# Kernel optimization log

Measured on AMD Instinct MI355X. Metric: run time of the kernel, lower is better.

## Reference

```python
import jax, jax.numpy as jnp
import numpy as np

T = 32            # num_tsteps
B = 8192          # batch_size
W_IN0, W_OUT0 = 36, 18
W_IN1, W_OUT1 = 18, 8
TILE0, TILE1 = 2, 1
BETA = (0.95, 0.95)
TH = (0.55, 0.25)
Q = 15000.0       # sephia mrr_Q
ER_DB = 20.0      # sephia extinction ratio
IL_DB = 0.0       # sephia insertion loss
SHIFT_PM = -250.0 # sephia resonance shift per unit spike
P_UNITY = 1e-4    # dbm_to_watt(-10): optical power per WDM channel at unit input


def _lif(inp, mem, beta, th):
    # snntorch Leaky, reset_mechanism='zero', reset_delay=True:
    # reset decided from incoming mem, membrane zeroed before leak+integrate.
    reset = (mem > th).astype(inp.dtype)
    mem_new = (beta * mem + inp) * (1.0 - reset)
    spk = (mem_new > th).astype(inp.dtype)
    return spk, mem_new


def _allpass(spk, wl_nm):
    # All-pass MRR modulator: spike shifts the ring resonance by SHIFT_PM.
    # Normalized detuning delta = shift / (FWHM/2), FWHM = lambda / Q.
    fwhm_pm = wl_nm * 1e3 / Q                      # [C]
    delta = (spk * SHIFT_PM) / (0.5 * fwhm_pm)     # [B, C]
    gamma = 10.0 ** (-ER_DB / 20.0)                # on-resonance amplitude (ER)
    il = 10.0 ** (-IL_DB / 20.0)                   # insertion loss factor
    return (il * (1j * delta + gamma) / (1j * delta + 1.0)).astype(jnp.complex64)


def setup_inputs() -> dict:
    key = jax.random.key(0)
    ks = jax.random.split(key, 6)
    return {
        "x_in": jax.random.uniform(ks[0], (T, B, W_IN0), jnp.float32),
        "W0": jax.random.uniform(ks[1], (TILE0, W_IN0 // TILE0, W_OUT0 * 2 // TILE0), jnp.float32),
        "d0": jax.random.normal(ks[2], (TILE0, W_OUT0 // TILE0), jnp.float32) * 5e3,
        "W1": jax.random.uniform(ks[3], (TILE1, W_IN1 // TILE1, W_OUT1 * 2 // TILE1), jnp.float32),
        "d1": jax.random.normal(ks[4], (TILE1, W_OUT1 // TILE1), jnp.float32) * 5e3,
        "peak_powers_dbm": jax.random.uniform(ks[5], (W_IN0,), jnp.float32, -15.0, -5.0),
    }


def reference(x_in, W0, d0, W1, d1, peak_powers_dbm):
    wl0 = 1550.0 + 0.8 * jnp.arange(W_OUT0, dtype=jnp.float32)   # MRR resonance wavelengths (nm)
    # sephia_inputs: sqrt(dbm_to_watt(P_dbm) * 1e6) field amplitude per channel
    amp0 = jnp.sqrt((10.0 ** (peak_powers_dbm[:W_OUT0] / 10.0) / 1000.0) * 1e6)
    S0 = W_OUT0 * 2 // TILE0   # 18 spatial channels after EO broadcast
    S1 = W_OUT1 * 2 // TILE1   # 16 spatial channels into layer 1

    def step(carry, x_t):
        mem0, mem1 = carry
        b = x_t.shape[0]
        # --- EO conversion + layer 0 MRR weight bank (power domain) ---
        p_in = x_t * P_UNITY                                     # [B, 36] optical power
        p0 = jnp.broadcast_to(p_in[:, :, None], (b, W_IN0, S0)).reshape(b, TILE0, W_IN0 // TILE0, S0)
        I0 = jnp.einsum('btws,tws->bts', p0, W0)                 # photocurrents [B,2,18]
        cur0 = ((I0[..., 0::2] - I0[..., 1::2]) * d0).reshape(b, W_OUT0)  # balanced PDs + Diagonal
        spk0, mem0 = _lif(cur0, mem0, BETA[0], TH[0])
        # --- SEPhIA all-pass MRR modulation of comb lines ---
        lo = _allpass(spk0, wl0) * amp0.astype(jnp.complex64)    # [B, 18] complex field
        pw0 = jnp.abs(lo) ** 2                                   # detected power == spike record
        # --- post-SEPhIA broadcast + layer 1 weight bank ---
        p1 = jnp.broadcast_to(pw0[:, :, None], (b, W_IN1, S1)).reshape(b, TILE1, W_IN1 // TILE1, S1)
        I1 = jnp.einsum('btws,tws->bts', p1, W1)                 # [B,1,16]
        cur1 = ((I1[..., 0::2] - I1[..., 1::2]) * d1).reshape(b, W_OUT1)
        spk1, mem1 = _lif(cur1, mem1, BETA[1], TH[1])
        return (mem0, mem1), (pw0, spk1, mem0, mem1)

    mem0 = jnp.zeros((x_in.shape[1], W_OUT0), x_in.dtype)
    mem1 = jnp.zeros((x_in.shape[1], W_OUT1), x_in.dtype)
    _, (spks0, spks1, mems0, mems1) = jax.lax.scan(step, (mem0, mem1), x_in)
    return spks0, spks1, mems0, mems1
```

## Files before the change

kernel.cpp:

```cpp
#include <hip/hip_runtime.h>


namespace {
constexpr int Tn = 32;
constexpr int Bn = 8192;
constexpr int O_PW = 0;
constexpr int O_S1 = Tn * Bn * 18;
constexpr int O_M0 = O_S1 + Tn * Bn * 8;
constexpr int O_M1 = O_M0 + Tn * Bn * 18;
}

__global__ __launch_bounds__(256, 4)
void oesnn_kernel(const float* __restrict__ x_in,
                  const float* __restrict__ W0g,
                  const float* __restrict__ d0g,
                  const float* __restrict__ W1g,
                  const float* __restrict__ d1g,
                  const float* __restrict__ peakg,
                  float* __restrict__ out)
{
    const int lt  = threadIdx.x & 63;
    const int tid = blockIdx.x * 256 + threadIdx.x;
    const int b   = tid >> 5;
    const int g   = tid & 31;
    const bool isL0 = (g < 18);
    const bool isL1 = (g >= 18) && (g < 26);

    float wA[18], wB[18];
    float dd = 0.f, pon = 0.f, poff = 0.f;
    int tl = 0;

    if (isL0) {
        tl = g / 9;
        const int jc = g % 9;
        dd = d0g[tl * 9 + jc];
        #pragma unroll
        for (int w = 0; w < 18; ++w) {
            const float2 p = *(const float2*)(W0g + ((tl * 18 + w) * 18 + 2 * jc));
            wA[w] = p.x;
            wB[w] = p.y;
        }
        const int c = g;
        const float wl    = 1550.0f + 0.8f * (float)c;
        const float halfw = 0.5f * (wl * 1e3f / 15000.0f);
        const float amp   = sqrtf((exp10f(peakg[c] / 10.0f) / 1000.0f) * 1e6f);
        {
            const float lr = 0.1f * amp;
            const float a  = sqrtf(lr * lr);
            poff = a * a;
        }
        {
            const float delta = -250.0f / halfw;
            const float den = fmaf(delta, delta, 1.0f);
            const float qr  = fmaf(delta, delta, 0.1f) / den;
            const float qi  = (delta - 0.1f * delta) / den;
            const float lr = qr * amp, li = qi * amp;
            const float a  = sqrtf(fmaf(lr, lr, li * li));
            pon = a * a;
        }
    } else {
        const int o = (g < 26) ? (g - 18) : 7;
        dd = d1g[o];
        #pragma unroll
        for (int w = 0; w < 18; ++w) {
            const float2 p = *(const float2*)(W1g + w * 16 + 2 * o);
            wA[w] = p.x;
            wB[w] = p.y;
        }
    }

    float mem0 = 0.f;
    float mem1 = 0.f;

    const float* xp = x_in + (size_t)b * 36 + tl * 18;
    float* opw = out + O_PW + (size_t)b * 18 + g;
    float* om0 = out + O_M0 + (size_t)b * 18 + g;
    const int o1 = isL1 ? (g - 18) : 0;
    float* os1 = out + O_S1 + (size_t)b * 8 + o1;
    float* om1 = out + O_M1 + (size_t)b * 8 + o1;

    float2 xv[9];
    #pragma unroll
    for (int k = 0; k < 9; ++k) xv[k] = *(const float2*)(xp + 2 * k);

    const int basel = lt & ~31;

    #pragma unroll 1
    for (int t = 0; t < Tn; ++t) {
        float se = 0.f, so = 0.f;
        #pragma unroll
        for (int k = 0; k < 9; ++k) {
            const float pa = xv[k].x * 1e-4f;
            se = fmaf(pa, wA[2 * k], se);
            so = fmaf(pa, wB[2 * k], so);
            const float pb = xv[k].y * 1e-4f;
            se = fmaf(pb, wA[2 * k + 1], se);
            so = fmaf(pb, wB[2 * k + 1], so);
        }

        xp += Bn * 36;
        if (t < Tn - 1) {
            #pragma unroll
            for (int k = 0; k < 9; ++k) xv[k] = *(const float2*)(xp + 2 * k);
        }

        const float c0 = (se - so) * dd;
        const float m2 = (mem0 > 0.55f) ? 0.0f : fmaf(0.95f, mem0, c0);
        mem0 = m2;
        const float pw = (m2 > 0.55f) ? pon : poff;

        if (isL0) {
            *opw = pw;
            *om0 = m2;
        }

        float i1e = 0.f, i1o = 0.f;
        #pragma unroll
        for (int c = 0; c < 18; ++c) {
            const float gp = __shfl(pw, basel + c, 64);
            i1e = fmaf(gp, wA[c], i1e);
            i1o = fmaf(gp, wB[c], i1o);
        }

        const float c1 = (i1e - i1o) * dd;
        const float m3 = (mem1 > 0.25f) ? 0.0f : fmaf(0.95f, mem1, c1);
        mem1 = m3;
        if (isL1) {
            *os1 = (m3 > 0.25f) ? 1.0f : 0.0f;
            *om1 = m3;
        }

        opw += Bn * 18;
        om0 += Bn * 18;
        os1 += Bn * 8;
        om1 += Bn * 8;
    }
}

extern "C" void kernel_launch(void* const* d_in, const int* in_sizes, int n_in,
                              void* d_out, int out_size, void* d_ws, size_t ws_size,
                              hipStream_t stream) {
    (void)in_sizes; (void)n_in; (void)out_size; (void)d_ws; (void)ws_size;
    const float* x  = (const float*)d_in[0];
    const float* W0 = (const float*)d_in[1];
    const float* d0 = (const float*)d_in[2];
    const float* W1 = (const float*)d_in[3];
    const float* d1 = (const float*)d_in[4];
    const float* pk = (const float*)d_in[5];
    float* out = (float*)d_out;

    dim3 grid(Bn * 32 / 256), block(256);
    hipLaunchKernelGGL(oesnn_kernel, grid, block, 0, stream,
                       x, W0, d0, W1, d1, pk, out);
}
```

Measured before the change: 135.6 us.

## Pipeline layer-1 one timestep behind layer-0 in a single per-lane dot product

Each lane now runs only its own layer's LIF. Layer-0 lanes handle the current timestep while layer-1 lanes handle the previous timestep, using spike powers shuffled into a register array in the prior iteration. This replaces the two dot products every lane computed per step with one shared, branch-free path, and unifies the store code. In exchange the loop runs one extra iteration, layer-1 lanes still issue unused x loads, and lanes 26-31 redundantly write duplicate layer-1 outputs.

```diff
diff --git a/kernel.cpp b/kernel.cpp
--- a/kernel.cpp
+++ b/kernel.cpp
@@ -23,22 +23,21 @@
     const int tid = blockIdx.x * 256 + threadIdx.x;
     const int b   = tid >> 5;
     const int g   = tid & 31;
-    const bool isL0 = (g < 18);
-    const bool isL1 = (g >= 18) && (g < 26);
+    const bool l0 = (g < 18);
+    const int  o  = l0 ? 0 : ((g < 26) ? (g - 18) : (g - 26));
+    const int  tl = l0 ? (g / 9) : 0;
 
     float wA[18], wB[18];
-    float dd = 0.f, pon = 0.f, poff = 0.f;
-    int tl = 0;
-
-    if (isL0) {
-        tl = g / 9;
+    float dd, hi, lo, th;
+    if (l0) {
         const int jc = g % 9;
         dd = d0g[tl * 9 + jc];
+        th = 0.55f;
         #pragma unroll
         for (int w = 0; w < 18; ++w) {
-            const float2 p = *(const float2*)(W0g + ((tl * 18 + w) * 18 + 2 * jc));
-            wA[w] = p.x;
-            wB[w] = p.y;
+            const float2 pr = *(const float2*)(W0g + ((tl * 18 + w) * 18 + 2 * jc));
+            wA[w] = pr.x;
+            wB[w] = pr.y;
         }
         const int c = g;
         const float wl    = 1550.0f + 0.8f * (float)c;
@@ -47,7 +46,7 @@
         {
             const float lr = 0.1f * amp;
             const float a  = sqrtf(lr * lr);
-            poff = a * a;
+            lo = a * a;
         }
         {
             const float delta = -250.0f / halfw;
@@ -56,84 +55,75 @@
             const float qi  = (delta - 0.1f * delta) / den;
             const float lr = qr * amp, li = qi * amp;
             const float a  = sqrtf(fmaf(lr, lr, li * li));
-            pon = a * a;
+            hi = a * a;
         }
     } else {
-        const int o = (g < 26) ? (g - 18) : 7;
         dd = d1g[o];
+        th = 0.25f;
+        hi = 1.0f;
+        lo = 0.0f;
         #pragma unroll
         for (int w = 0; w < 18; ++w) {
-            const float2 p = *(const float2*)(W1g + w * 16 + 2 * o);
-            wA[w] = p.x;
-            wB[w] = p.y;
+            const float2 pr = *(const float2*)(W1g + w * 16 + 2 * o);
+            wA[w] = pr.x;
+            wB[w] = pr.y;
         }
     }
 
-    float mem0 = 0.f;
-    float mem1 = 0.f;
+    float mem = 0.f;
 
     const float* xp = x_in + (size_t)b * 36 + tl * 18;
-    float* opw = out + O_PW + (size_t)b * 18 + g;
-    float* om0 = out + O_M0 + (size_t)b * 18 + g;
-    const int o1 = isL1 ? (g - 18) : 0;
-    float* os1 = out + O_S1 + (size_t)b * 8 + o1;
-    float* om1 = out + O_M1 + (size_t)b * 8 + o1;
+    float* pa = l0 ? (out + O_PW + (size_t)b * 18 + g)
+                   : (out + O_S1 + (size_t)b * 8 + o - (size_t)Bn * 8);
+    float* pb = l0 ? (out + O_M0 + (size_t)b * 18 + g)
+                   : (out + O_M1 + (size_t)b * 8 + o - (size_t)Bn * 8);
+    const int strA = l0 ? (Bn * 18) : (Bn * 8);
 
     float2 xv[9];
     #pragma unroll
     for (int k = 0; k < 9; ++k) xv[k] = *(const float2*)(xp + 2 * k);
 
-    const int basel = lt & ~31;
+    float pwall[18];
+    #pragma unroll
+    for (int c = 0; c < 18; ++c) pwall[c] = 0.f;
+
+    const int base32 = lt & ~31;
 
     #pragma unroll 1
-    for (int t = 0; t < Tn; ++t) {
+    for (int tt = 0; tt <= Tn; ++tt) {
         float se = 0.f, so = 0.f;
         #pragma unroll
         for (int k = 0; k < 9; ++k) {
-            const float pa = xv[k].x * 1e-4f;
-            se = fmaf(pa, wA[2 * k], se);
-            so = fmaf(pa, wB[2 * k], so);
-            const float pb = xv[k].y * 1e-4f;
-            se = fmaf(pb, wA[2 * k + 1], se);
-            so = fmaf(pb, wB[2 * k + 1], so);
+            const float ua = l0 ? (xv[k].x * 1e-4f) : pwall[2 * k];
+            se = fmaf(ua, wA[2 * k], se);
+            so = fmaf(ua, wB[2 * k], so);
+            const float ub = l0 ? (xv[k].y * 1e-4f) : pwall[2 * k + 1];
+            se = fmaf(ub, wA[2 * k + 1], se);
+            so = fmaf(ub, wB[2 * k + 1], so);
         }
 
-        xp += Bn * 36;
-        if (t < Tn - 1) {
+        if (tt + 1 < Tn) {
+            xp += Bn * 36;
             #pragma unroll
             for (int k = 0; k < 9; ++k) xv[k] = *(const float2*)(xp + 2 * k);
         }
 
-        const float c0 = (se - so) * dd;
-        const float m2 = (mem0 > 0.55f) ? 0.0f : fmaf(0.95f, mem0, c0);
-        mem0 = m2;
-        const float pw = (m2 > 0.55f) ? pon : poff;
+        const float cc = (se - so) * dd;
+        const float m2 = (mem > th) ? 0.0f : fmaf(0.95f, mem, cc);
+        mem = m2;
+        const float ov = (m2 > th) ? hi : lo;
 
-        if (isL0) {
-            *opw = pw;
-            *om0 = m2;
+        #pragma unroll
+        for (int c = 0; c < 18; ++c)
+            pwall[c] = __shfl(ov, base32 + c, 64);
+
+        const bool en = l0 ? (tt < Tn) : (tt > 0);
+        if (en) {
+            *pa = ov;
+            *pb = m2;
         }
-
-        float i1e = 0.f, i1o = 0.f;
-        #pragma unroll
-        for (int c = 0; c < 18; ++c) {
-            const float gp = __shfl(pw, basel + c, 64);
-            i1e = fmaf(gp, wA[c], i1e);
-            i1o = fmaf(gp, wB[c], i1o);
-        }
-
-        const float c1 = (i1e - i1o) * dd;
-        const float m3 = (mem1 > 0.25f) ? 0.0f : fmaf(0.95f, mem1, c1);
-        mem1 = m3;
-        if (isL1) {
-            *os1 = (m3 > 0.25f) ? 1.0f : 0.0f;
-            *om1 = m3;
-        }
-
-        opw += Bn * 18;
-        om0 += Bn * 18;
-        os1 += Bn * 8;
-        om1 += Bn * 8;
+        pa += strA;
+        pb += strA;
     }
 }
 
```

After: 133.0 us. No clear change (-1.9%).
